# Performance work log

Hardware: AMD Instinct MI355X
Metric: run time of the kernel (lower is better)

The kernel has to match this reference:

```python
import jax, jax.numpy as jnp
import numpy as np

DIM = 512
HEADS = 8
DIM_HEAD = 64
HIDDEN = HEADS * DIM_HEAD
SCALE = DIM_HEAD ** -0.5


def rmsnorm_ch(x, g):
    # F.normalize over channel dim (axis=1), then * g * sqrt(C)
    # x: [b, c, l], g: [c]
    n = jnp.maximum(jnp.linalg.norm(x, axis=1, keepdims=True), 1e-12)
    c = x.shape[1]
    return (x / n) * g[None, :, None] * (c ** 0.5)


def setup_inputs() -> dict:
    key = jax.random.key(0)
    ks = jax.random.split(key, 6)
    b, l = 8, 4096
    x = jax.random.normal(ks[0], (b, DIM, l), dtype=jnp.float32)
    g_in = jnp.ones((DIM,), dtype=jnp.float32)
    # conv1d kernel_size=1 == matmul; kaiming-ish init scale
    w_qkv = jax.random.normal(ks[1], (3 * HIDDEN, DIM), dtype=jnp.float32) * (1.0 / np.sqrt(DIM))
    w_out = jax.random.normal(ks[2], (DIM, HIDDEN), dtype=jnp.float32) * (1.0 / np.sqrt(HIDDEN))
    b_out = jax.random.normal(ks[3], (DIM,), dtype=jnp.float32) * 0.01
    g_out = jnp.ones((DIM,), dtype=jnp.float32)
    return {"x": x, "g_in": g_in, "w_qkv": w_qkv, "w_out": w_out, "b_out": b_out, "g_out": g_out}


def reference(x, g_in, w_qkv, w_out, b_out, g_out):
    b, c, l = x.shape
    residual = x
    xn = rmsnorm_ch(x, g_in)                       # [b, c, l]
    qkv = jnp.einsum('oc,bcl->bol', w_qkv, xn)     # [b, 3*hidden, l]
    q, k, v = jnp.split(qkv, 3, axis=1)            # each [b, hidden, l]
    def to_heads(t):
        return t.reshape(b, HEADS, DIM_HEAD, l)    # [b, h, d, l]
    q, k, v = to_heads(q), to_heads(k), to_heads(v)
    q = jax.nn.softmax(q, axis=2) * SCALE          # softmax over head-dim d
    k = jax.nn.softmax(k, axis=3)                  # softmax over sequence l
    context = jnp.einsum('bhdn,bhen->bhde', k, v)  # [b, h, d, e]
    out = jnp.einsum('bhde,bhdn->bhen', context, q)  # [b, h, e, l]
    out = out.reshape(b, HIDDEN, l)
    o = jnp.einsum('ch,bhl->bcl', w_out, out) + b_out[None, :, None]
    o = rmsnorm_ch(o, g_out)
    return o + residual
```

## Files before the change

### kernel.cpp

```cpp
#include <hip/hip_runtime.h>


#define BB 8
#define CC 512
#define LL 4096
#define HH 8
#define DH 64
#define TC 1536

__device__ __constant__ const float SQRT_C = 22.62741699796952f;
#define SCALE_Q 0.125f

typedef unsigned short bfr_t;
typedef __attribute__((ext_vector_type(8))) short short8;
typedef __attribute__((ext_vector_type(4))) float f32x4;

__device__ __forceinline__ float bf2f(bfr_t v) {
  union { unsigned u; float f; } c; c.u = ((unsigned)v) << 16; return c.f;
}
__device__ __forceinline__ bfr_t f2bf(float f) {
  union { float f; unsigned u; } c; c.f = f;
  unsigned u = c.u + 0x7fffu + ((c.u >> 16) & 1u);
  return (bfr_t)(u >> 16);
}

__device__ __forceinline__ void load_lds16(const bfr_t* g, short* l) {
  __builtin_amdgcn_global_load_lds(
      (const __attribute__((address_space(1))) void*)g,
      (__attribute__((address_space(3))) void*)l, 16, 0, 0);
}

__global__ __launch_bounds__(256) void conv_bf16(const float* __restrict__ in,
                                                 bfr_t* __restrict__ out, int n) {
  int i = blockIdx.x * 256 + threadIdx.x;
  if (i < n) out[i] = f2bf(in[i]);
}

__global__ __launch_bounds__(256) void colnorm(const float* __restrict__ x,
                                               float* __restrict__ norms) {
  __shared__ float red[4][64];
  int b = blockIdx.y, l0 = blockIdx.x * 64;
  int t = threadIdx.x, ll = t & 63, cg = t >> 6;
  const float* xb = x + (size_t)b * CC * LL + l0 + ll;
  float ss = 0.f;
  for (int c = cg * 128; c < cg * 128 + 128; ++c) {
    float v = xb[(size_t)c * LL];
    ss += v * v;
  }
  red[cg][ll] = ss;
  __syncthreads();
  if (cg == 0) {
    float s = red[0][ll] + red[1][ll] + red[2][ll] + red[3][ll];
    norms[(size_t)b * LL + l0 + ll] = fmaxf(sqrtf(s), 1e-12f);
  }
}

__global__ __launch_bounds__(256) void norm_transpose(
    const float* __restrict__ x, const float* __restrict__ g,
    const float* __restrict__ norms, bfr_t* __restrict__ xt) {
  __shared__ float tile[64][65];
  int b = blockIdx.z, c0 = blockIdx.y * 64, l0 = blockIdx.x * 64;
  int t = threadIdx.x;
  const float* xb = x + (size_t)b * CC * LL;
#pragma unroll
  for (int i = 0; i < 16; ++i) {
    int idx = i * 256 + t;
    int c = idx >> 6, l = idx & 63;
    tile[c][l] = xb[(size_t)(c0 + c) * LL + l0 + l];
  }
  __syncthreads();
  int l = t >> 2, cc = (t & 3) * 16;
  float invn = SQRT_C / norms[(size_t)b * LL + l0 + l];
  union { short s[16]; f32x4 v[2]; } pk;
#pragma unroll
  for (int u = 0; u < 16; ++u) {
    int c = cc + u;
    pk.s[u] = (short)f2bf(tile[c][l] * g[c0 + c] * invn);
  }
  bfr_t* dst = xt + ((size_t)b * LL + l0 + l) * CC + c0 + cc;
  *(f32x4*)dst = pk.v[0];
  *(f32x4*)(dst + 8) = pk.v[1];
}

__global__ __launch_bounds__(256) void gemm_bf16(
    const bfr_t* __restrict__ A, const bfr_t* __restrict__ Bt,
    bfr_t* __restrict__ Cout, const float* __restrict__ bias, int M) {
  const int K = 512;
  __shared__ short As[128 * 64];
  __shared__ short Bs[128 * 64];
  int b = blockIdx.z;
  int m0 = blockIdx.y * 128, n0 = blockIdx.x * 128;
  int t = threadIdx.x, lane = t & 63, wid = t >> 6;
  int wm = wid & 1, wn = wid >> 1;
  int quad = lane >> 4, r = lane & 15, r7 = r & 7;
  const bfr_t* Bbase = Bt + (size_t)b * LL * K;

  int lrow = lane >> 3;
  int lgran = (lane & 7) ^ lrow;
  const bfr_t* gA[4];
  const bfr_t* gB[4];
  short* lA[4];
  short* lB[4];
#pragma unroll
  for (int u = 0; u < 4; ++u) {
    int ch = wid * 4 + u;
    int row = ch * 8 + lrow;
    gA[u] = A + (size_t)(m0 + row) * K + lgran * 8;
    gB[u] = Bbase + (size_t)(n0 + row) * K + lgran * 8;
    lA[u] = As + ch * 512;
    lB[u] = Bs + ch * 512;
  }

  f32x4 acc[4][4] = {};

  for (int k0 = 0; k0 < K; k0 += 64) {
    __syncthreads();
#pragma unroll
    for (int u = 0; u < 4; ++u) {
      load_lds16(gA[u] + k0, lA[u]);
      load_lds16(gB[u] + k0, lB[u]);
    }
    __syncthreads();
#pragma unroll
    for (int ks = 0; ks < 2; ++ks) {
      short8 af[4], bfr8[4];
#pragma unroll
      for (int i = 0; i < 4; ++i) {
        int ga = ((ks * 4 + quad) ^ r7) * 8;
        af[i]   = *(const short8*)&As[(wm * 64 + i * 16 + r) * 64 + ga];
        bfr8[i] = *(const short8*)&Bs[(wn * 64 + i * 16 + r) * 64 + ga];
      }
#pragma unroll
      for (int i = 0; i < 4; ++i)
#pragma unroll
        for (int j = 0; j < 4; ++j)
          acc[i][j] = __builtin_amdgcn_mfma_f32_16x16x32_bf16(af[i], bfr8[j],
                                                              acc[i][j], 0, 0, 0);
    }
  }

  bfr_t* Cb = Cout + (size_t)b * M * LL;
#pragma unroll
  for (int i = 0; i < 4; ++i) {
#pragma unroll
    for (int reg = 0; reg < 4; ++reg) {
      int row = m0 + wm * 64 + i * 16 + quad * 4 + reg;
      float bi = bias ? bias[row] : 0.f;
#pragma unroll
      for (int j = 0; j < 4; ++j) {
        int col = n0 + wn * 64 + j * 16 + r;
        Cb[(size_t)row * LL + col] = f2bf(acc[i][j][reg] + bi);
      }
    }
  }
}

__global__ __launch_bounds__(256) void kstats(bfr_t* __restrict__ qkv,
                                              float* __restrict__ ksum) {
  __shared__ float red[256];
  int row = blockIdx.x;
  int b = row >> 9, hd = row & 511;
  bfr_t* kr = qkv + ((size_t)b * TC + 512 + hd) * LL;
  int t = threadIdx.x;
  float vals[16];
  float m = -1e30f;
#pragma unroll
  for (int i = 0; i < 16; ++i) {
    float v = bf2f(kr[t + i * 256]);
    vals[i] = v;
    m = fmaxf(m, v);
  }
  red[t] = m;
  __syncthreads();
  for (int s = 128; s > 0; s >>= 1) {
    if (t < s) red[t] = fmaxf(red[t], red[t + s]);
    __syncthreads();
  }
  m = red[0];
  __syncthreads();
  float ss = 0.f;
#pragma unroll
  for (int i = 0; i < 16; ++i) {
    bfr_t eb = f2bf(__expf(vals[i] - m));
    kr[t + i * 256] = eb;
    ss += bf2f(eb);
  }
  red[t] = ss;
  __syncthreads();
  for (int s = 128; s > 0; s >>= 1) {
    if (t < s) red[t] += red[t + s];
    __syncthreads();
  }
  if (t == 0) ksum[row] = red[0];
}

__global__ __launch_bounds__(256) void context_mfma(
    const bfr_t* __restrict__ qkv, float* __restrict__ ctx_p) {
  __shared__ float red[4][4096];
  int s = blockIdx.x, bh = blockIdx.y;
  int b = bh >> 3, h = bh & 7;
  int t = threadIdx.x, lane = t & 63, wid = t >> 6;
  int quad = lane >> 4, r = lane & 15;
  const bfr_t* kb = qkv + ((size_t)b * TC + 512 + h * 64) * LL;
  const bfr_t* vb = qkv + ((size_t)b * TC + 1024 + h * 64) * LL;
  int n_base = s * 512 + wid * 128;
  f32x4 acc[4][4] = {};
#pragma unroll
  for (int ks = 0; ks < 4; ++ks) {
    int n0 = n_base + ks * 32;
    short8 af[4], bf8[4];
#pragma unroll
    for (int i = 0; i < 4; ++i) {
      af[i]  = *(const short8*)&kb[(size_t)(i * 16 + r) * LL + n0 + quad * 8];
      bf8[i] = *(const short8*)&vb[(size_t)(i * 16 + r) * LL + n0 + quad * 8];
    }
#pragma unroll
    for (int i = 0; i < 4; ++i)
#pragma unroll
      for (int j = 0; j < 4; ++j)
        acc[i][j] = __builtin_amdgcn_mfma_f32_16x16x32_bf16(af[i], bf8[j],
                                                            acc[i][j], 0, 0, 0);
  }
#pragma unroll
  for (int i = 0; i < 4; ++i)
#pragma unroll
    for (int j = 0; j < 4; ++j)
#pragma unroll
      for (int reg = 0; reg < 4; ++reg)
        red[wid][(i * 16 + quad * 4 + reg) * 64 + j * 16 + r] = acc[i][j][reg];
  __syncthreads();
  float* out = ctx_p + ((size_t)bh * 8 + s) * 4096;
#pragma unroll
  for (int u = 0; u < 16; ++u) {
    int idx = u * 256 + t;
    out[idx] = red[0][idx] + red[1][idx] + red[2][idx] + red[3][idx];
  }
}

__global__ __launch_bounds__(256) void context_reduce(
    const float* __restrict__ ctx_p, const float* __restrict__ ksum,
    bfr_t* __restrict__ ctx_bf) {
  int bh = blockIdx.x;
  int b = bh >> 3, h = bh & 7;
  int t = threadIdx.x;
#pragma unroll
  for (int i = 0; i < 16; ++i) {
    int idx = i * 256 + t;
    int d = idx >> 6;
    float sum = 0.f;
#pragma unroll
    for (int s = 0; s < 8; ++s) sum += ctx_p[((size_t)bh * 8 + s) * 4096 + idx];
    ctx_bf[(size_t)bh * 4096 + idx] = f2bf(sum / ksum[b * 512 + h * 64 + d]);
  }
}

__global__ __launch_bounds__(256) void qsoftmax(bfr_t* __restrict__ qkv) {
  int b = blockIdx.z, h = blockIdx.y;
  int n = blockIdx.x * 256 + threadIdx.x;
  const bfr_t* qb = qkv + ((size_t)b * TC + h * 64) * LL + n;
  float v[64];
  float m = -1e30f;
#pragma unroll
  for (int d = 0; d < 64; ++d) {
    v[d] = bf2f(qb[(size_t)d * LL]);
    m = fmaxf(m, v[d]);
  }
  float ssum = 0.f;
#pragma unroll
  for (int d = 0; d < 64; ++d) {
    v[d] = __expf(v[d] - m);
    ssum += v[d];
  }
  float sc = SCALE_Q / ssum;
  bfr_t* dst = qkv + ((size_t)b * TC + 512) * LL + ((size_t)h * LL + n) * 64;
#pragma unroll
  for (int g8 = 0; g8 < 8; ++g8) {
    union { short s[8]; f32x4 f; } pk;
#pragma unroll
    for (int u = 0; u < 8; ++u) pk.s[u] = (short)f2bf(v[g8 * 8 + u] * sc);
    *(f32x4*)(dst + g8 * 8) = pk.f;
  }
}

__global__ __launch_bounds__(256) void apply_mfma(
    const bfr_t* __restrict__ qkv, const bfr_t* __restrict__ ctx_bf,
    bfr_t* __restrict__ out_t) {
  int b = blockIdx.z, h = blockIdx.y;
  int t = threadIdx.x, lane = t & 63, wid = t >> 6;
  int quad = lane >> 4, r = lane & 15;
  int n0 = blockIdx.x * 256 + wid * 64;
  const bfr_t* qs = qkv + ((size_t)b * TC + 512) * LL + (size_t)h * LL * 64;
  const bfr_t* cb = ctx_bf + (size_t)(b * HH + h) * 4096;
  short8 bfrag[2][4];
#pragma unroll
  for (int ks = 0; ks < 2; ++ks)
#pragma unroll
    for (int j = 0; j < 4; ++j) {
      union { short s[8]; short8 v; } u;
#pragma unroll
      for (int jj = 0; jj < 8; ++jj)
        u.s[jj] = (short)cb[(ks * 32 + quad * 8 + jj) * 64 + j * 16 + r];
      bfrag[ks][j] = u.v;
    }
  f32x4 acc[4][4] = {};
#pragma unroll
  for (int ks = 0; ks < 2; ++ks) {
    short8 af[4];
#pragma unroll
    for (int i = 0; i < 4; ++i)
      af[i] = *(const short8*)&qs[(size_t)(n0 + i * 16 + r) * 64 + ks * 32 + quad * 8];
#pragma unroll
    for (int i = 0; i < 4; ++i)
#pragma unroll
      for (int j = 0; j < 4; ++j)
        acc[i][j] = __builtin_amdgcn_mfma_f32_16x16x32_bf16(af[i], bfrag[ks][j],
                                                            acc[i][j], 0, 0, 0);
  }
  bfr_t* dst = out_t + (size_t)b * LL * 512 + h * 64;
#pragma unroll
  for (int i = 0; i < 4; ++i)
#pragma unroll
    for (int reg = 0; reg < 4; ++reg) {
      int row = n0 + i * 16 + quad * 4 + reg;
#pragma unroll
      for (int j = 0; j < 4; ++j)
        dst[(size_t)row * 512 + j * 16 + r] = f2bf(acc[i][j][reg]);
    }
}

__global__ __launch_bounds__(256) void final_norm_res(
    const bfr_t* __restrict__ o, const float* __restrict__ g,
    const float* __restrict__ x, float* __restrict__ out) {
  __shared__ float red[4][64];
  __shared__ float invn[64];
  int b = blockIdx.y, l0 = blockIdx.x * 64;
  int t = threadIdx.x, ll = t & 63, cg = t >> 6;
  const bfr_t* ob = o + (size_t)b * CC * LL + l0 + ll;
  float ss = 0.f;
  for (int c = cg * 128; c < cg * 128 + 128; ++c) {
    float v = bf2f(ob[(size_t)c * LL]);
    ss += v * v;
  }
  red[cg][ll] = ss;
  __syncthreads();
  if (cg == 0) {
    float s = red[0][ll] + red[1][ll] + red[2][ll] + red[3][ll];
    invn[ll] = SQRT_C / fmaxf(sqrtf(s), 1e-12f);
  }
  __syncthreads();
  float iv = invn[ll];
  const float* xb = x + (size_t)b * CC * LL + l0 + ll;
  float* outb = out + (size_t)b * CC * LL + l0 + ll;
  for (int c = cg * 128; c < cg * 128 + 128; ++c) {
    float v = bf2f(ob[(size_t)c * LL]);
    outb[(size_t)c * LL] = v * g[c] * iv + xb[(size_t)c * LL];
  }
}

extern "C" void kernel_launch(void* const* d_in, const int* in_sizes, int n_in,
                              void* d_out, int out_size, void* d_ws,
                              size_t ws_size, hipStream_t stream) {
  const float* x     = (const float*)d_in[0];
  const float* g_in  = (const float*)d_in[1];
  const float* w_qkv = (const float*)d_in[2];
  const float* w_out = (const float*)d_in[3];
  const float* b_out = (const float*)d_in[4];
  const float* g_out = (const float*)d_in[5];
  float* out = (float*)d_out;

  char* ws = (char*)d_ws;
  const size_t off_wqkv  = 0;
  const size_t off_wout  = 1572864;
  const size_t off_norms = 2097152;
  const size_t off_ksum  = 2244608;
  const size_t off_ctx   = 2260992;
  const size_t off_ctxp  = 3309568;
  const size_t off_xt    = 11698176;
  const size_t off_qkv   = 45252608;
  const size_t ws_need   = 145915904;
  if (ws_size < ws_need) return;

  bfr_t* wqkv_bf = (bfr_t*)(ws + off_wqkv);
  bfr_t* wout_bf = (bfr_t*)(ws + off_wout);
  float* norms   = (float*)(ws + off_norms);
  float* ksum    = (float*)(ws + off_ksum);
  bfr_t* ctx_bf  = (bfr_t*)(ws + off_ctx);
  float* ctxp    = (float*)(ws + off_ctxp);
  bfr_t* xt      = (bfr_t*)(ws + off_xt);
  bfr_t* qkv     = (bfr_t*)(ws + off_qkv);
  bfr_t* o_bf    = (bfr_t*)(ws + off_qkv);

  conv_bf16<<<dim3((1536 * 512 + 255) / 256), 256, 0, stream>>>(w_qkv, wqkv_bf, 1536 * 512);
  conv_bf16<<<dim3((512 * 512 + 255) / 256), 256, 0, stream>>>(w_out, wout_bf, 512 * 512);
  colnorm<<<dim3(LL / 64, BB), 256, 0, stream>>>(x, norms);
  norm_transpose<<<dim3(LL / 64, CC / 64, BB), 256, 0, stream>>>(x, g_in, norms, xt);
  gemm_bf16<<<dim3(LL / 128, TC / 128, BB), 256, 0, stream>>>(wqkv_bf, xt, qkv, nullptr, TC);
  kstats<<<dim3(BB * 512), 256, 0, stream>>>(qkv, ksum);
  context_mfma<<<dim3(8, BB * HH), 256, 0, stream>>>(qkv, ctxp);
  context_reduce<<<dim3(BB * HH), 256, 0, stream>>>(ctxp, ksum, ctx_bf);
  qsoftmax<<<dim3(LL / 256, HH, BB), 256, 0, stream>>>(qkv);
  apply_mfma<<<dim3(LL / 256, HH, BB), 256, 0, stream>>>(qkv, ctx_bf, xt);
  gemm_bf16<<<dim3(LL / 128, CC / 128, BB), 256, 0, stream>>>(wout_bf, xt, o_bf, b_out, CC);
  final_norm_res<<<dim3(LL / 64, BB), 256, 0, stream>>>(o_bf, g_out, x, out);
}
```

Measured before the change: 335.7 us.

## Fuse colnorm with transpose, move k-exp into context, fuse q-softmax into apply

Merges the column-norm and normalize-transpose kernels into one pass that holds each 64-column strip of x in registers, so x is read once instead of twice. kstats no longer writes exp(k) back; it stores the row max and sum, and context_mfma recomputes exp on the fly. The q softmax is folded into the apply kernel using cross-lane shuffles, which removes a kernel and a bf16 round trip. The costs are heavy register use (128 floats per thread in the norm kernel), less grid parallelism there, and strided uncoalesced q loads in apply.

```diff
diff --git a/kernel.cpp b/kernel.cpp
--- a/kernel.cpp
+++ b/kernel.cpp
@@ -36,50 +36,54 @@
   if (i < n) out[i] = f2bf(in[i]);
 }
 
-__global__ __launch_bounds__(256) void colnorm(const float* __restrict__ x,
-                                               float* __restrict__ norms) {
+__global__ __launch_bounds__(256) void fused_norm_transpose(
+    const float* __restrict__ x, const float* __restrict__ g,
+    bfr_t* __restrict__ xt) {
+  __shared__ float tile[64][65];
   __shared__ float red[4][64];
+  __shared__ float invn_s[64];
   int b = blockIdx.y, l0 = blockIdx.x * 64;
   int t = threadIdx.x, ll = t & 63, cg = t >> 6;
-  const float* xb = x + (size_t)b * CC * LL + l0 + ll;
+  const float* xb = x + (size_t)b * CC * LL + l0;
+  float vals[8][16];
   float ss = 0.f;
-  for (int c = cg * 128; c < cg * 128 + 128; ++c) {
-    float v = xb[(size_t)c * LL];
-    ss += v * v;
+#pragma unroll
+  for (int ch = 0; ch < 8; ++ch) {
+    int c0 = ch * 64;
+#pragma unroll
+    for (int i = 0; i < 16; ++i) {
+      int c = i * 4 + cg;
+      float v = xb[(size_t)(c0 + c) * LL + ll];
+      vals[ch][i] = v;
+      ss += v * v;
+    }
   }
   red[cg][ll] = ss;
   __syncthreads();
   if (cg == 0) {
     float s = red[0][ll] + red[1][ll] + red[2][ll] + red[3][ll];
-    norms[(size_t)b * LL + l0 + ll] = fmaxf(sqrtf(s), 1e-12f);
-  }
-}
-
-__global__ __launch_bounds__(256) void norm_transpose(
-    const float* __restrict__ x, const float* __restrict__ g,
-    const float* __restrict__ norms, bfr_t* __restrict__ xt) {
-  __shared__ float tile[64][65];
-  int b = blockIdx.z, c0 = blockIdx.y * 64, l0 = blockIdx.x * 64;
-  int t = threadIdx.x;
-  const float* xb = x + (size_t)b * CC * LL;
-#pragma unroll
-  for (int i = 0; i < 16; ++i) {
-    int idx = i * 256 + t;
-    int c = idx >> 6, l = idx & 63;
-    tile[c][l] = xb[(size_t)(c0 + c) * LL + l0 + l];
-  }
-  __syncthreads();
-  int l = t >> 2, cc = (t & 3) * 16;
-  float invn = SQRT_C / norms[(size_t)b * LL + l0 + l];
-  union { short s[16]; f32x4 v[2]; } pk;
-#pragma unroll
-  for (int u = 0; u < 16; ++u) {
-    int c = cc + u;
-    pk.s[u] = (short)f2bf(tile[c][l] * g[c0 + c] * invn);
-  }
-  bfr_t* dst = xt + ((size_t)b * LL + l0 + l) * CC + c0 + cc;
-  *(f32x4*)dst = pk.v[0];
-  *(f32x4*)(dst + 8) = pk.v[1];
+    invn_s[ll] = SQRT_C / fmaxf(sqrtf(s), 1e-12f);
+  }
+  __syncthreads();
+  int lw = t >> 2, ccw = (t & 3) * 16;
+  float iv = invn_s[lw];
+#pragma unroll
+  for (int ch = 0; ch < 8; ++ch) {
+    int c0 = ch * 64;
+#pragma unroll
+    for (int i = 0; i < 16; ++i) tile[i * 4 + cg][ll] = vals[ch][i];
+    __syncthreads();
+    union { short s[16]; f32x4 v[2]; } pk;
+#pragma unroll
+    for (int u = 0; u < 16; ++u) {
+      int c = ccw + u;
+      pk.s[u] = (short)f2bf(tile[c][lw] * g[c0 + c] * iv);
+    }
+    bfr_t* dst = xt + ((size_t)b * LL + l0 + lw) * CC + c0 + ccw;
+    *(f32x4*)dst = pk.v[0];
+    *(f32x4*)(dst + 8) = pk.v[1];
+    __syncthreads();
+  }
 }
 
 __global__ __launch_bounds__(256) void gemm_bf16(
@@ -155,12 +159,13 @@
   }
 }
 
-__global__ __launch_bounds__(256) void kstats(bfr_t* __restrict__ qkv,
+__global__ __launch_bounds__(256) void kstats(const bfr_t* __restrict__ qkv,
+                                              float* __restrict__ kmax,
                                               float* __restrict__ ksum) {
   __shared__ float red[256];
   int row = blockIdx.x;
   int b = row >> 9, hd = row & 511;
-  bfr_t* kr = qkv + ((size_t)b * TC + 512 + hd) * LL;
+  const bfr_t* kr = qkv + ((size_t)b * TC + 512 + hd) * LL;
   int t = threadIdx.x;
   float vals[16];
   float m = -1e30f;
@@ -180,22 +185,19 @@
   __syncthreads();
   float ss = 0.f;
 #pragma unroll
-  for (int i = 0; i < 16; ++i) {
-    bfr_t eb = f2bf(__expf(vals[i] - m));
-    kr[t + i * 256] = eb;
-    ss += bf2f(eb);
-  }
+  for (int i = 0; i < 16; ++i) ss += __expf(vals[i] - m);
   red[t] = ss;
   __syncthreads();
   for (int s = 128; s > 0; s >>= 1) {
     if (t < s) red[t] += red[t + s];
     __syncthreads();
   }
-  if (t == 0) ksum[row] = red[0];
+  if (t == 0) { kmax[row] = m; ksum[row] = red[0]; }
 }
 
 __global__ __launch_bounds__(256) void context_mfma(
-    const bfr_t* __restrict__ qkv, float* __restrict__ ctx_p) {
+    const bfr_t* __restrict__ qkv, const float* __restrict__ kmax,
+    float* __restrict__ ctx_p) {
   __shared__ float red[4][4096];
   int s = blockIdx.x, bh = blockIdx.y;
   int b = bh >> 3, h = bh & 7;
@@ -203,6 +205,9 @@
   int quad = lane >> 4, r = lane & 15;
   const bfr_t* kb = qkv + ((size_t)b * TC + 512 + h * 64) * LL;
   const bfr_t* vb = qkv + ((size_t)b * TC + 1024 + h * 64) * LL;
+  float km[4];
+#pragma unroll
+  for (int i = 0; i < 4; ++i) km[i] = kmax[b * 512 + h * 64 + i * 16 + r];
   int n_base = s * 512 + wid * 128;
   f32x4 acc[4][4] = {};
 #pragma unroll
@@ -211,7 +216,12 @@
     short8 af[4], bf8[4];
 #pragma unroll
     for (int i = 0; i < 4; ++i) {
-      af[i]  = *(const short8*)&kb[(size_t)(i * 16 + r) * LL + n0 + quad * 8];
+      union { short s[8]; short8 v8; } uk;
+      uk.v8 = *(const short8*)&kb[(size_t)(i * 16 + r) * LL + n0 + quad * 8];
+#pragma unroll
+      for (int jj = 0; jj < 8; ++jj)
+        uk.s[jj] = (short)f2bf(__expf(bf2f((bfr_t)uk.s[jj]) - km[i]));
+      af[i] = uk.v8;
       bf8[i] = *(const short8*)&vb[(size_t)(i * 16 + r) * LL + n0 + quad * 8];
     }
 #pragma unroll
@@ -254,68 +264,79 @@
   }
 }
 
-__global__ __launch_bounds__(256) void qsoftmax(bfr_t* __restrict__ qkv) {
-  int b = blockIdx.z, h = blockIdx.y;
-  int n = blockIdx.x * 256 + threadIdx.x;
-  const bfr_t* qb = qkv + ((size_t)b * TC + h * 64) * LL + n;
-  float v[64];
-  float m = -1e30f;
-#pragma unroll
-  for (int d = 0; d < 64; ++d) {
-    v[d] = bf2f(qb[(size_t)d * LL]);
-    m = fmaxf(m, v[d]);
-  }
-  float ssum = 0.f;
-#pragma unroll
-  for (int d = 0; d < 64; ++d) {
-    v[d] = __expf(v[d] - m);
-    ssum += v[d];
-  }
-  float sc = SCALE_Q / ssum;
-  bfr_t* dst = qkv + ((size_t)b * TC + 512) * LL + ((size_t)h * LL + n) * 64;
-#pragma unroll
-  for (int g8 = 0; g8 < 8; ++g8) {
-    union { short s[8]; f32x4 f; } pk;
-#pragma unroll
-    for (int u = 0; u < 8; ++u) pk.s[u] = (short)f2bf(v[g8 * 8 + u] * sc);
-    *(f32x4*)(dst + g8 * 8) = pk.f;
-  }
-}
-
-__global__ __launch_bounds__(256) void apply_mfma(
+__global__ __launch_bounds__(256) void apply_fused(
     const bfr_t* __restrict__ qkv, const bfr_t* __restrict__ ctx_bf,
     bfr_t* __restrict__ out_t) {
   int b = blockIdx.z, h = blockIdx.y;
   int t = threadIdx.x, lane = t & 63, wid = t >> 6;
   int quad = lane >> 4, r = lane & 15;
   int n0 = blockIdx.x * 256 + wid * 64;
-  const bfr_t* qs = qkv + ((size_t)b * TC + 512) * LL + (size_t)h * LL * 64;
+  const bfr_t* qb = qkv + ((size_t)b * TC + h * 64) * LL;
   const bfr_t* cb = ctx_bf + (size_t)(b * HH + h) * 4096;
+  float v[4][16];
+  float pm[4];
+#pragma unroll
+  for (int i = 0; i < 4; ++i) {
+    pm[i] = -1e30f;
+#pragma unroll
+    for (int ks = 0; ks < 2; ++ks)
+#pragma unroll
+      for (int jj = 0; jj < 8; ++jj) {
+        float q = bf2f(qb[(size_t)(ks * 32 + quad * 8 + jj) * LL + n0 + i * 16 + r]);
+        v[i][ks * 8 + jj] = q;
+        pm[i] = fmaxf(pm[i], q);
+      }
+  }
+#pragma unroll
+  for (int i = 0; i < 4; ++i) {
+    pm[i] = fmaxf(pm[i], __shfl_xor(pm[i], 16, 64));
+    pm[i] = fmaxf(pm[i], __shfl_xor(pm[i], 32, 64));
+  }
+  float psum[4];
+#pragma unroll
+  for (int i = 0; i < 4; ++i) {
+    float s = 0.f;
+#pragma unroll
+    for (int u = 0; u < 16; ++u) { v[i][u] = __expf(v[i][u] - pm[i]); s += v[i][u]; }
+    psum[i] = s;
+  }
+#pragma unroll
+  for (int i = 0; i < 4; ++i) {
+    psum[i] += __shfl_xor(psum[i], 16, 64);
+    psum[i] += __shfl_xor(psum[i], 32, 64);
+  }
+  short8 af[2][4];
+#pragma unroll
+  for (int i = 0; i < 4; ++i) {
+    float sc = SCALE_Q / psum[i];
+#pragma unroll
+    for (int ks = 0; ks < 2; ++ks) {
+      union { short s[8]; short8 v8; } u;
+#pragma unroll
+      for (int jj = 0; jj < 8; ++jj) u.s[jj] = (short)f2bf(v[i][ks * 8 + jj] * sc);
+      af[ks][i] = u.v8;
+    }
+  }
   short8 bfrag[2][4];
 #pragma unroll
   for (int ks = 0; ks < 2; ++ks)
 #pragma unroll
     for (int j = 0; j < 4; ++j) {
-      union { short s[8]; short8 v; } u;
+      union { short s[8]; short8 v8; } u;
 #pragma unroll
       for (int jj = 0; jj < 8; ++jj)
         u.s[jj] = (short)cb[(ks * 32 + quad * 8 + jj) * 64 + j * 16 + r];
-      bfrag[ks][j] = u.v;
+      bfrag[ks][j] = u.v8;
     }
   f32x4 acc[4][4] = {};
 #pragma unroll
-  for (int ks = 0; ks < 2; ++ks) {
-    short8 af[4];
+  for (int ks = 0; ks < 2; ++ks)
 #pragma unroll
     for (int i = 0; i < 4; ++i)
-      af[i] = *(const short8*)&qs[(size_t)(n0 + i * 16 + r) * 64 + ks * 32 + quad * 8];
-#pragma unroll
-    for (int i = 0; i < 4; ++i)
 #pragma unroll
       for (int j = 0; j < 4; ++j)
-        acc[i][j] = __builtin_amdgcn_mfma_f32_16x16x32_bf16(af[i], bfrag[ks][j],
+        acc[i][j] = __builtin_amdgcn_mfma_f32_16x16x32_bf16(af[ks][i], bfrag[ks][j],
                                                             acc[i][j], 0, 0, 0);
-  }
   bfr_t* dst = out_t + (size_t)b * LL * 512 + h * 64;
 #pragma unroll
   for (int i = 0; i < 4; ++i)
@@ -371,7 +392,7 @@
   char* ws = (char*)d_ws;
   const size_t off_wqkv  = 0;
   const size_t off_wout  = 1572864;
-  const size_t off_norms = 2097152;
+  const size_t off_kmax  = 2097152;
   const size_t off_ksum  = 2244608;
   const size_t off_ctx   = 2260992;
   const size_t off_ctxp  = 3309568;
@@ -382,7 +403,7 @@
 
   bfr_t* wqkv_bf = (bfr_t*)(ws + off_wqkv);
   bfr_t* wout_bf = (bfr_t*)(ws + off_wout);
-  float* norms   = (float*)(ws + off_norms);
+  float* kmax    = (float*)(ws + off_kmax);
   float* ksum    = (float*)(ws + off_ksum);
   bfr_t* ctx_bf  = (bfr_t*)(ws + off_ctx);
   float* ctxp    = (float*)(ws + off_ctxp);
@@ -392,14 +413,12 @@
 
   conv_bf16<<<dim3((1536 * 512 + 255) / 256), 256, 0, stream>>>(w_qkv, wqkv_bf, 1536 * 512);
   conv_bf16<<<dim3((512 * 512 + 255) / 256), 256, 0, stream>>>(w_out, wout_bf, 512 * 512);
-  colnorm<<<dim3(LL / 64, BB), 256, 0, stream>>>(x, norms);
-  norm_transpose<<<dim3(LL / 64, CC / 64, BB), 256, 0, stream>>>(x, g_in, norms, xt);
+  fused_norm_transpose<<<dim3(LL / 64, BB), 256, 0, stream>>>(x, g_in, xt);
   gemm_bf16<<<dim3(LL / 128, TC / 128, BB), 256, 0, stream>>>(wqkv_bf, xt, qkv, nullptr, TC);
-  kstats<<<dim3(BB * 512), 256, 0, stream>>>(qkv, ksum);
-  context_mfma<<<dim3(8, BB * HH), 256, 0, stream>>>(qkv, ctxp);
+  kstats<<<dim3(BB * 512), 256, 0, stream>>>(qkv, kmax, ksum);
+  context_mfma<<<dim3(8, BB * HH), 256, 0, stream>>>(qkv, kmax, ctxp);
   context_reduce<<<dim3(BB * HH), 256, 0, stream>>>(ctxp, ksum, ctx_bf);
-  qsoftmax<<<dim3(LL / 256, HH, BB), 256, 0, stream>>>(qkv);
-  apply_mfma<<<dim3(LL / 256, HH, BB), 256, 0, stream>>>(qkv, ctx_bf, xt);
+  apply_fused<<<dim3(LL / 256, HH, BB), 256, 0, stream>>>(qkv, ctx_bf, xt);
   gemm_bf16<<<dim3(LL / 128, CC / 128, BB), 256, 0, stream>>>(wout_bf, xt, o_bf, b_out, CC);
   final_norm_res<<<dim3(LL / 64, BB), 256, 0, stream>>>(o_bf, g_out, x, out);
 }
```

After: 310.7 us. 7.5% less time.
